# Kernel tuning notes

Measured on AMD Instinct MI355X. Metric: run time of the kernel, lower is better.

## Reference

```python
import jax, jax.numpy as jnp
import numpy as np

B, T, N = 8, 128, 64
K, d = 8, 64
D = K * d  # 512
NEG = -32767.0  # -2**15 + 1, as in the torch module


def _xavier(key, shape):
    fan_out, fan_in = shape
    limit = float(np.sqrt(6.0 / (fan_in + fan_out)))
    return jax.random.uniform(key, shape, jnp.float32, -limit, limit)


def setup_inputs() -> dict:
    key = jax.random.key(0)
    ks = jax.random.split(key, 6)
    X = jax.random.normal(ks[0], (B, T, N, D), jnp.float32)
    STE = jax.random.normal(ks[1], (B, T, N, 2 * D), jnp.float32)
    Wq = _xavier(ks[2], (D, 3 * D))
    Wk = _xavier(ks[3], (D, 3 * D))
    Wv = _xavier(ks[4], (D, 3 * D))
    Wo = _xavier(ks[5], (D, D))
    bq = jnp.zeros((D,), jnp.float32)
    bk = jnp.zeros((D,), jnp.float32)
    bv = jnp.zeros((D,), jnp.float32)
    bo = jnp.zeros((D,), jnp.float32)
    return {"X": X, "STE": STE, "Wq": Wq, "bq": bq, "Wk": Wk, "bk": bk,
            "Wv": Wv, "bv": bv, "Wo": Wo, "bo": bo}


def _fc(H, W, b):
    # 1x1 conv over channel dim == linear on last axis, then ReLU
    return jax.nn.relu(jnp.einsum('btnc,oc->btno', H, W) + b)


def _split_heads(x):
    # [B,T,N,D] -> [K,B,N,T,d]; torch splits last dim into K chunks of d and
    # stacks them along the batch dim (head-major), then permutes (0,2,1,3).
    return x.reshape(B, T, N, K, d).transpose(3, 0, 2, 1, 4)


def reference(X, STE, Wq, bq, Wk, bk, Wv, bv, Wo, bo):
    H = jnp.concatenate([X, STE], axis=-1)  # [B,T,N,3D]
    q = _split_heads(_fc(H, Wq, bq))  # [K,B,N,T,d]
    k = _split_heads(_fc(H, Wk, bk))
    v = _split_heads(_fc(H, Wv, bv))
    att = jnp.einsum('kbntd,kbnsd->kbnts', q, k) / jnp.sqrt(jnp.float32(d))
    causal = jnp.tril(jnp.ones((T, T), bool))  # [T,T]
    att = jnp.where(causal, att, NEG)
    att = jax.nn.softmax(att, axis=-1)
    out = jnp.einsum('kbnts,kbnsd->kbntd', att, v)  # [K,B,N,T,d]
    out = out.transpose(1, 3, 2, 0, 4).reshape(B, T, N, D)  # heads back to channels
    return jax.nn.relu(jnp.einsum('btnc,oc->btno', out, Wo) + bo)
```

## Files before the change

kernel.cpp:

```cpp
#include <hip/hip_runtime.h>
#include <hip/hip_bf16.h>


typedef __attribute__((ext_vector_type(8))) short short8;
typedef __attribute__((ext_vector_type(8))) _Float16 half8;
typedef __attribute__((ext_vector_type(4))) float floatx4;
typedef __attribute__((ext_vector_type(4))) unsigned int uintx4;

static __device__ __forceinline__ ushort f2b(float f) {
  __hip_bfloat16 h = __float2bfloat16(f);
  return __builtin_bit_cast(ushort, h);
}
static __device__ __forceinline__ ushort f2h(float f) {
  _Float16 h = (_Float16)f;
  return __builtin_bit_cast(ushort, h);
}
static __device__ __forceinline__ float blo(unsigned int w) {
  return __builtin_bit_cast(float, w << 16);
}
static __device__ __forceinline__ float bhi(unsigned int w) {
  return __builtin_bit_cast(float, w & 0xffff0000u);
}
static __device__ __forceinline__ uintx4 cvt8(const float* __restrict__ p) {
  const floatx4 f0 = *(const floatx4*)(p);
  const floatx4 f1 = *(const floatx4*)(p + 4);
  uintx4 r;
  r[0] = (unsigned int)f2b(f0[0]) | ((unsigned int)f2b(f0[1]) << 16);
  r[1] = (unsigned int)f2b(f0[2]) | ((unsigned int)f2b(f0[3]) << 16);
  r[2] = (unsigned int)f2b(f1[0]) | ((unsigned int)f2b(f1[1]) << 16);
  r[3] = (unsigned int)f2b(f1[2]) | ((unsigned int)f2b(f1[3]) << 16);
  return r;
}

template<int KDIM, bool CONCAT, bool TRIPLE, bool A_BF16, bool OUT_F32>
__global__ __launch_bounds__(256, 2)
void gemm_relu_bt(const void* __restrict__ A0v, const void* __restrict__ A1v,
                  const float* __restrict__ W0, const float* __restrict__ W1,
                  const float* __restrict__ W2,
                  const float* __restrict__ bias0, const float* __restrict__ bias1,
                  const float* __restrict__ bias2,
                  void* __restrict__ Cv, int ldc)
{
  __shared__ ushort As[128 * 72];
  __shared__ ushort Bs[128 * 72];

  const int tn = blockIdx.x, tm = blockIdx.y;
  const int tid = threadIdx.x;
  const int wave = tid >> 6, lane = tid & 63;
  const int quad = lane >> 4, lid = lane & 15;
  const int wm = wave >> 1, wn = wave & 1;

  const float* W; const float* bias; int nbase, cbase;
  if (TRIPLE) {
    const int seg = tn >> 2;
    W    = (seg == 0) ? W0 : (seg == 1) ? W1 : W2;
    bias = (seg == 0) ? bias0 : (seg == 1) ? bias1 : bias2;
    nbase = (tn & 3) * 128;
    cbase = seg * 512;
  } else { W = W0; bias = bias0; nbase = tn * 128; cbase = 0; }

  floatx4 acc[4][4];
#pragma unroll
  for (int i = 0; i < 4; i++)
#pragma unroll
    for (int j = 0; j < 4; j++) acc[i][j] = (floatx4){0.f, 0.f, 0.f, 0.f};

  for (int kt = 0; kt < KDIM / 64; ++kt) {
#pragma unroll
    for (int i = 0; i < 4; i++) {
      const int cidx = tid + i * 256;
      const int row = cidx >> 3, ch = cidx & 7;
      const int k0 = kt * 64 + ch * 8;
      uintx4 va, vb;
      if (A_BF16) {
        const ushort* A0 = (const ushort*)A0v;
        va = *(const uintx4*)(A0 + (size_t)(tm * 128 + row) * KDIM + k0);
      } else if (CONCAT) {
        const int m = tm * 128 + row;
        if (k0 < 512) va = cvt8((const float*)A0v + (size_t)m * 512 + k0);
        else          va = cvt8((const float*)A1v + (size_t)m * 1024 + (k0 - 512));
      } else {
        va = cvt8((const float*)A0v + (size_t)(tm * 128 + row) * KDIM + k0);
      }
      vb = cvt8(W + (size_t)(nbase + row) * KDIM + k0);
      *(uintx4*)(&As[row * 72 + ch * 8]) = va;
      *(uintx4*)(&Bs[row * 72 + ch * 8]) = vb;
    }
    __syncthreads();
#pragma unroll
    for (int ks = 0; ks < 2; ++ks) {
      short8 af[4], bfr[4];
#pragma unroll
      for (int t = 0; t < 4; t++) {
        af[t]  = *(const short8*)(&As[(wm * 64 + t * 16 + lid) * 72 + ks * 32 + quad * 8]);
        bfr[t] = *(const short8*)(&Bs[(wn * 64 + t * 16 + lid) * 72 + ks * 32 + quad * 8]);
      }
#pragma unroll
      for (int i = 0; i < 4; i++)
#pragma unroll
        for (int j = 0; j < 4; j++)
          acc[i][j] = __builtin_amdgcn_mfma_f32_16x16x32_bf16(af[i], bfr[j], acc[i][j], 0, 0, 0);
    }
    __syncthreads();
  }

#pragma unroll
  for (int j = 0; j < 4; j++) {
    const int ncol = nbase + wn * 64 + j * 16 + lid;
    const float bv = bias[ncol];
    const int cg = cbase + ncol;
#pragma unroll
    for (int i = 0; i < 4; i++) {
      const int mrow = tm * 128 + wm * 64 + i * 16 + quad * 4;
#pragma unroll
      for (int r = 0; r < 4; r++) {
        float v = acc[i][j][r] + bv;
        v = v > 0.f ? v : 0.f;
        if (OUT_F32) ((float*)Cv)[(size_t)(mrow + r) * ldc + cg] = v;
        else         ((ushort*)Cv)[(size_t)(mrow + r) * ldc + cg] = f2b(v);
      }
    }
  }
}

__global__ __launch_bounds__(256, 2)
void attn_mfma(const ushort* __restrict__ qkv, ushort* __restrict__ outb)
{
  __shared__ ushort Ks[128 * 64];
  __shared__ ushort Vt[64 * 128];
  __shared__ ushort Ps[128 * 128];

  const int bx = blockIdx.x;
  const int head = bx >> 9;
  const int b = (bx >> 6) & 7;
  const int n = bx & 63;
  const int tid = threadIdx.x;
  const int wave = tid >> 6, lane = tid & 63;
  const int quad = lane >> 4, lid = lane & 15;

  char* KsB = (char*)Ks;
  char* VtB = (char*)Vt;
  char* PsB = (char*)Ps;

#pragma unroll
  for (int i = 0; i < 4; i++) {
    const int idx = tid + i * 256;
    const int s = idx >> 3, slot = idx & 7;
    const ushort* gb = qkv + ((size_t)((b * 128 + s) * 64 + n)) * 1536 + head * 64;
    const uintx4 kw = *(const uintx4*)(gb + 512 + slot * 8);
    *(uintx4*)(KsB + s * 128 + ((slot ^ (s & 7)) << 4)) = kw;
    const uintx4 vw = *(const uintx4*)(gb + 1024 + slot * 8);
#pragma unroll
    for (int j = 0; j < 4; j++) {
      const int d0 = slot * 8 + 2 * j;
      const int d1 = d0 + 1;
      *(ushort*)(VtB + d0 * 256 + (((s >> 3) ^ (d0 & 15)) << 4) + (s & 7) * 2) = f2h(blo(vw[j]));
      *(ushort*)(VtB + d1 * 256 + (((s >> 3) ^ (d1 & 15)) << 4) + (s & 7) * 2) = f2h(bhi(vw[j]));
    }
  }

  short8 qf[2][2];
#pragma unroll
  for (int i = 0; i < 2; i++)
#pragma unroll
    for (int ks = 0; ks < 2; ks++) {
      const int t = wave * 32 + i * 16 + lid;
      qf[i][ks] = *(const short8*)(qkv + ((size_t)((b * 128 + t) * 64 + n)) * 1536
                                   + head * 64 + ks * 32 + quad * 8);
    }
  __syncthreads();

  floatx4 acc[2][8];
#pragma unroll
  for (int i = 0; i < 2; i++)
#pragma unroll
    for (int j = 0; j < 8; j++) acc[i][j] = (floatx4){0.f, 0.f, 0.f, 0.f};

#pragma unroll
  for (int ks = 0; ks < 2; ks++) {
#pragma unroll
    for (int j = 0; j < 8; j++) {
      const int srow = j * 16 + lid;
      const short8 kf = *(const short8*)(KsB + srow * 128
                                         + (((ks * 4 + quad) ^ (srow & 7)) << 4));
#pragma unroll
      for (int i = 0; i < 2; i++)
        acc[i][j] = __builtin_amdgcn_mfma_f32_16x16x32_bf16(qf[i][ks], kf, acc[i][j], 0, 0, 0);
    }
  }

  float sum[2][4];
#pragma unroll
  for (int i = 0; i < 2; i++)
#pragma unroll
    for (int r = 0; r < 4; r++) {
      const int row = wave * 32 + i * 16 + quad * 4 + r;
      float m = -1e30f;
#pragma unroll
      for (int j = 0; j < 8; j++) {
        const int col = j * 16 + lid;
        float sv = acc[i][j][r] * 0.125f;
        sv = (col > row) ? -1e30f : sv;
        acc[i][j][r] = sv;
        m = fmaxf(m, sv);
      }
      m = fmaxf(m, __shfl_xor(m, 1));
      m = fmaxf(m, __shfl_xor(m, 2));
      m = fmaxf(m, __shfl_xor(m, 4));
      m = fmaxf(m, __shfl_xor(m, 8));
      float s = 0.f;
#pragma unroll
      for (int j = 0; j < 8; j++) {
        const float p = __expf(acc[i][j][r] - m);
        s += p;
        const int col = j * 16 + lid;
        *(ushort*)(PsB + row * 256 + (((col >> 3) ^ (row & 15)) << 4) + (col & 7) * 2) = f2h(p);
      }
      s += __shfl_xor(s, 1);
      s += __shfl_xor(s, 2);
      s += __shfl_xor(s, 4);
      s += __shfl_xor(s, 8);
      sum[i][r] = s;
    }
  __syncthreads();

  floatx4 acc2[2][4];
#pragma unroll
  for (int i = 0; i < 2; i++)
#pragma unroll
    for (int j2 = 0; j2 < 4; j2++) acc2[i][j2] = (floatx4){0.f, 0.f, 0.f, 0.f};

#pragma unroll
  for (int ks2 = 0; ks2 < 4; ks2++) {
    short8 pf[2];
#pragma unroll
    for (int i = 0; i < 2; i++) {
      const int row = wave * 32 + i * 16 + lid;
      pf[i] = *(const short8*)(PsB + row * 256 + (((ks2 * 4 + quad) ^ (row & 15)) << 4));
    }
#pragma unroll
    for (int j2 = 0; j2 < 4; j2++) {
      const int dd = j2 * 16 + lid;
      const short8 vf = *(const short8*)(VtB + dd * 256 + (((ks2 * 4 + quad) ^ (dd & 15)) << 4));
#pragma unroll
      for (int i = 0; i < 2; i++)
        acc2[i][j2] = __builtin_amdgcn_mfma_f32_16x16x32_f16(
            __builtin_bit_cast(half8, pf[i]), __builtin_bit_cast(half8, vf),
            acc2[i][j2], 0, 0, 0);
    }
  }

#pragma unroll
  for (int i = 0; i < 2; i++)
#pragma unroll
    for (int r = 0; r < 4; r++) {
      const float inv = 1.f / sum[i][r];
      const int t = wave * 32 + i * 16 + quad * 4 + r;
      ushort* ob = outb + ((size_t)((b * 128 + t) * 64 + n)) * 512 + head * 64;
#pragma unroll
      for (int j2 = 0; j2 < 4; j2++)
        ob[j2 * 16 + lid] = f2b(acc2[i][j2][r] * inv);
    }
}

extern "C" void kernel_launch(void* const* d_in, const int* in_sizes, int n_in,
                              void* d_out, int out_size, void* d_ws, size_t ws_size,
                              hipStream_t stream) {
  const float* X   = (const float*)d_in[0];
  const float* STE = (const float*)d_in[1];
  const float* Wq  = (const float*)d_in[2];
  const float* bq  = (const float*)d_in[3];
  const float* Wk  = (const float*)d_in[4];
  const float* bk  = (const float*)d_in[5];
  const float* Wv  = (const float*)d_in[6];
  const float* bv  = (const float*)d_in[7];
  const float* Wo  = (const float*)d_in[8];
  const float* bo  = (const float*)d_in[9];
  float* out = (float*)d_out;

  ushort* qkv = (ushort*)d_ws;
  ushort* att = qkv + (size_t)65536 * 1536;

  gemm_relu_bt<1536, true, true, false, false><<<dim3(12, 512), 256, 0, stream>>>(
      X, STE, Wq, Wk, Wv, bq, bk, bv, qkv, 1536);
  attn_mfma<<<dim3(4096), 256, 0, stream>>>(qkv, att);
  gemm_relu_bt<512, false, false, true, true><<<dim3(4, 512), 256, 0, stream>>>(
      att, nullptr, Wo, nullptr, nullptr, bo, nullptr, nullptr, out, 512);
}
```

Measured before the change: 1.165 ms.

## Pre-convert inputs to bf16 and load GEMM tiles via async global-to-LDS

Adds a separate pass that converts X/STE (concatenated into H) and all weights to bf16 once, so the GEMM no longer re-reads and converts fp32 tiles on every block. The GEMM then loads tiles with global_load_lds directly into LDS, using an XOR-swizzled layout to avoid bank conflicts, and drops the padded rows. In exchange it writes and re-reads a large bf16 H buffer in workspace and launches one more kernel. Each of the 12 column tiles previously re-read and converted the fp32 A rows.

```diff
diff --git a/kernel.cpp b/kernel.cpp
--- a/kernel.cpp
+++ b/kernel.cpp
@@ -31,18 +31,55 @@
   r[3] = (unsigned int)f2b(f1[2]) | ((unsigned int)f2b(f1[3]) << 16);
   return r;
 }
-
-template<int KDIM, bool CONCAT, bool TRIPLE, bool A_BF16, bool OUT_F32>
+static __device__ __forceinline__ void gld_lds16(const ushort* g, ushort* l) {
+  __builtin_amdgcn_global_load_lds(
+      (const __attribute__((address_space(1))) void*)g,
+      (__attribute__((address_space(3))) void*)l, 16, 0, 0);
+}
+
+__global__ __launch_bounds__(256)
+void cvt_bf16_pass(const float* __restrict__ X, const float* __restrict__ STE,
+                   const float* __restrict__ Wq, const float* __restrict__ Wk,
+                   const float* __restrict__ Wv, const float* __restrict__ Wo,
+                   ushort* __restrict__ H, ushort* __restrict__ Wb,
+                   ushort* __restrict__ Wob)
+{
+  const int stride = gridDim.x * blockDim.x;
+  for (int c = blockIdx.x * blockDim.x + threadIdx.x; c < 12910592; c += stride) {
+    const float* src; ushort* dst;
+    if (c < 4194304) {
+      const int m = c >> 6, col = (c & 63) << 3;
+      src = X + ((size_t)c << 3);
+      dst = H + (size_t)m * 1536 + col;
+    } else if (c < 12582912) {
+      const int c2 = c - 4194304;
+      const int m = c2 >> 7, col = (c2 & 127) << 3;
+      src = STE + ((size_t)c2 << 3);
+      dst = H + (size_t)m * 1536 + 512 + col;
+    } else if (c < 12877824) {
+      const int c3 = c - 12582912;
+      const int w = c3 / 98304;
+      const int r = c3 - w * 98304;
+      const float* Ws = (w == 0) ? Wq : (w == 1) ? Wk : Wv;
+      src = Ws + ((size_t)r << 3);
+      dst = Wb + ((size_t)c3 << 3);
+    } else {
+      const int c4 = c - 12877824;
+      src = Wo + ((size_t)c4 << 3);
+      dst = Wob + ((size_t)c4 << 3);
+    }
+    *(uintx4*)dst = cvt8(src);
+  }
+}
+
+template<int KDIM, bool TRIPLE, bool OUT_F32>
 __global__ __launch_bounds__(256, 2)
-void gemm_relu_bt(const void* __restrict__ A0v, const void* __restrict__ A1v,
-                  const float* __restrict__ W0, const float* __restrict__ W1,
-                  const float* __restrict__ W2,
-                  const float* __restrict__ bias0, const float* __restrict__ bias1,
-                  const float* __restrict__ bias2,
-                  void* __restrict__ Cv, int ldc)
+void gemm_bf16_async(const ushort* __restrict__ A, const ushort* __restrict__ Wall,
+                     const float* __restrict__ b0, const float* __restrict__ b1,
+                     const float* __restrict__ b2, void* __restrict__ Cv, int ldc)
 {
-  __shared__ ushort As[128 * 72];
-  __shared__ ushort Bs[128 * 72];
+  __shared__ ushort As[128 * 64];
+  __shared__ ushort Bs[128 * 64];
 
   const int tn = blockIdx.x, tm = blockIdx.y;
   const int tid = threadIdx.x;
@@ -50,14 +87,16 @@
   const int quad = lane >> 4, lid = lane & 15;
   const int wm = wave >> 1, wn = wave & 1;
 
-  const float* W; const float* bias; int nbase, cbase;
+  const ushort* W; const float* bias; int nbase, cbase;
   if (TRIPLE) {
     const int seg = tn >> 2;
-    W    = (seg == 0) ? W0 : (seg == 1) ? W1 : W2;
-    bias = (seg == 0) ? bias0 : (seg == 1) ? bias1 : bias2;
+    W = Wall + (size_t)seg * 512 * 1536;
+    bias = (seg == 0) ? b0 : (seg == 1) ? b1 : b2;
     nbase = (tn & 3) * 128;
     cbase = seg * 512;
-  } else { W = W0; bias = bias0; nbase = tn * 128; cbase = 0; }
+  } else { W = Wall; bias = b0; nbase = tn * 128; cbase = 0; }
+
+  const int rloc = lane >> 3, sphys = lane & 7;
 
   floatx4 acc[4][4];
 #pragma unroll
@@ -65,26 +104,17 @@
 #pragma unroll
     for (int j = 0; j < 4; j++) acc[i][j] = (floatx4){0.f, 0.f, 0.f, 0.f};
 
+  const char* AsB = (const char*)As;
+  const char* BsB = (const char*)Bs;
+
   for (int kt = 0; kt < KDIM / 64; ++kt) {
 #pragma unroll
     for (int i = 0; i < 4; i++) {
-      const int cidx = tid + i * 256;
-      const int row = cidx >> 3, ch = cidx & 7;
-      const int k0 = kt * 64 + ch * 8;
-      uintx4 va, vb;
-      if (A_BF16) {
-        const ushort* A0 = (const ushort*)A0v;
-        va = *(const uintx4*)(A0 + (size_t)(tm * 128 + row) * KDIM + k0);
-      } else if (CONCAT) {
-        const int m = tm * 128 + row;
-        if (k0 < 512) va = cvt8((const float*)A0v + (size_t)m * 512 + k0);
-        else          va = cvt8((const float*)A1v + (size_t)m * 1024 + (k0 - 512));
-      } else {
-        va = cvt8((const float*)A0v + (size_t)(tm * 128 + row) * KDIM + k0);
-      }
-      vb = cvt8(W + (size_t)(nbase + row) * KDIM + k0);
-      *(uintx4*)(&As[row * 72 + ch * 8]) = va;
-      *(uintx4*)(&Bs[row * 72 + ch * 8]) = vb;
+      const int row = (wave * 4 + i) * 8 + rloc;
+      const int slog = sphys ^ (row & 7);
+      const int k0 = kt * 64 + slog * 8;
+      gld_lds16(A + (size_t)(tm * 128 + row) * KDIM + k0, As + (wave * 4 + i) * 512);
+      gld_lds16(W + (size_t)(nbase + row) * KDIM + k0,    Bs + (wave * 4 + i) * 512);
     }
     __syncthreads();
 #pragma unroll
@@ -92,8 +122,10 @@
       short8 af[4], bfr[4];
 #pragma unroll
       for (int t = 0; t < 4; t++) {
-        af[t]  = *(const short8*)(&As[(wm * 64 + t * 16 + lid) * 72 + ks * 32 + quad * 8]);
-        bfr[t] = *(const short8*)(&Bs[(wn * 64 + t * 16 + lid) * 72 + ks * 32 + quad * 8]);
+        const int ar = wm * 64 + t * 16 + lid;
+        const int br = wn * 64 + t * 16 + lid;
+        af[t]  = *(const short8*)(AsB + ar * 128 + (((ks * 4 + quad) ^ (ar & 7)) << 4));
+        bfr[t] = *(const short8*)(BsB + br * 128 + (((ks * 4 + quad) ^ (br & 7)) << 4));
       }
 #pragma unroll
       for (int i = 0; i < 4; i++)
@@ -279,11 +311,15 @@
   float* out = (float*)d_out;
 
   ushort* qkv = (ushort*)d_ws;
-  ushort* att = qkv + (size_t)65536 * 1536;
-
-  gemm_relu_bt<1536, true, true, false, false><<<dim3(12, 512), 256, 0, stream>>>(
-      X, STE, Wq, Wk, Wv, bq, bk, bv, qkv, 1536);
+  ushort* H   = qkv + (size_t)65536 * 1536;
+  ushort* att = H;
+  ushort* Wb  = H + (size_t)65536 * 1536;
+  ushort* Wob = Wb + (size_t)3 * 512 * 1536;
+
+  cvt_bf16_pass<<<2048, 256, 0, stream>>>(X, STE, Wq, Wk, Wv, Wo, H, Wb, Wob);
+  gemm_bf16_async<1536, true, false><<<dim3(12, 512), 256, 0, stream>>>(
+      H, Wb, bq, bk, bv, qkv, 1536);
   attn_mfma<<<dim3(4096), 256, 0, stream>>>(qkv, att);
-  gemm_relu_bt<512, false, false, true, true><<<dim3(4, 512), 256, 0, stream>>>(
-      att, nullptr, Wo, nullptr, nullptr, bo, nullptr, nullptr, out, 512);
-}
+  gemm_bf16_async<512, false, true><<<dim3(4, 512), 256, 0, stream>>>(
+      att, Wob, bo, nullptr, nullptr, out, 512);
+}
```

Measured after the change: 970.0 us. 1.2x faster.
